# Kernel optimization log

Hardware: AMD Instinct MI355X
Metric: run time of the kernel (lower is better)

## Reference

```python
import jax, jax.numpy as jnp
import numpy as np

B, S, D, H = 2, 2048, 1024, 16
DH = D // H  # 64
NEG = -1000000000.0


def setup_inputs() -> dict:
    key = jax.random.key(0)
    ks = jax.random.split(key, 10)
    scale = 1.0 / np.sqrt(D)
    inp = {
        "x": jax.random.normal(ks[0], (B, S, D), dtype=jnp.float32),
        "mask": jax.random.randint(ks[1], (B, S, S), 0, 2, dtype=jnp.int32),
        "Wq": jax.random.normal(ks[2], (D, D), dtype=jnp.float32) * scale,
        "bq": jnp.zeros((D,), dtype=jnp.float32),
        "Wk": jax.random.normal(ks[3], (D, D), dtype=jnp.float32) * scale,
        "bk": jnp.zeros((D,), dtype=jnp.float32),
        "Wv": jax.random.normal(ks[4], (D, D), dtype=jnp.float32) * scale,
        "bv": jnp.zeros((D,), dtype=jnp.float32),
        "Wo": jax.random.normal(ks[5], (D, D), dtype=jnp.float32) * scale,
        "bo": jnp.zeros((D,), dtype=jnp.float32),
    }
    return inp


def reference(x, mask, Wq, bq, Wk, bk, Wv, bv, Wo, bo):
    b, s, _ = x.shape
    # Linear projections (torch Linear: y = x @ W^T + b), then split heads -> [b,h,s,dh]
    q = (x @ Wq.T + bq).reshape(b, s, H, DH).transpose(0, 2, 1, 3)
    k = (x @ Wk.T + bk).reshape(b, s, H, DH).transpose(0, 2, 1, 3)
    v = (x @ Wv.T + bv).reshape(b, s, H, DH).transpose(0, 2, 1, 3)
    # scores: [b,h,sq,sk]
    scores = jnp.einsum("bhqd,bhkd->bhqk", q, k) / jnp.sqrt(jnp.float32(DH))
    # code masks where mask == 0 (mask broadcast over heads)
    scores = jnp.where(mask[:, None, :, :] == 0, NEG, scores)
    attn = jax.nn.softmax(scores, axis=-1)
    out = jnp.einsum("bhqk,bhkd->bhqd", attn, v)  # [b,h,sq,dh]
    out = out.transpose(0, 2, 1, 3).reshape(b, s, D)  # merge heads -> [b,s,d]
    return out @ Wo.T + bo
```

## Files before the change

### kernel.cpp

```cpp
#include <hip/hip_runtime.h>
#include <stdint.h>

#define SB 2
#define SS 2048
#define SD 1024
#define SH 16
#define SDH 64
#define SM (SB*SS)
#define NEGINF_MASK -1000000000.0f
#define QSCALE 0.18033688011112043f

typedef __attribute__((ext_vector_type(8))) short short8;
typedef __attribute__((ext_vector_type(4))) short short4v;
typedef __attribute__((ext_vector_type(4))) float f32x4;
typedef __attribute__((ext_vector_type(4))) float float4v;
typedef __attribute__((ext_vector_type(2))) uint32_t uint2v;

__device__ static inline short f2bf(float f) {
    uint32_t u = __float_as_uint(f);
    u += 0x7fffu + ((u >> 16) & 1u);
    return (short)(u >> 16);
}

__device__ static inline void gload_lds16(const void* g, void* l) {
    __builtin_amdgcn_global_load_lds(
        (__attribute__((address_space(1))) void*)g,
        (__attribute__((address_space(3))) void*)l,
        16, 0, 0);
}

#define NX4 (SM*SD/4)
#define NW4 (SD*SD/4)
__global__ void cvt_all_kernel(const float* __restrict__ x,
                               const float* __restrict__ Wq, const float* __restrict__ Wk,
                               const float* __restrict__ Wv, const float* __restrict__ Wo,
                               short* __restrict__ xb,
                               short* __restrict__ wqb, short* __restrict__ wkb,
                               short* __restrict__ wvb, short* __restrict__ wob) {
    int i = blockIdx.x * 256 + threadIdx.x;
    const float* src; short* dst; int idx;
    if (i < NX4) { src = x; dst = xb; idx = i; }
    else {
        int j = i - NX4;
        int sel = j >> 18;
        idx = j & (NW4 - 1);
        src = (sel == 0) ? Wq : (sel == 1) ? Wk : (sel == 2) ? Wv : Wo;
        dst = (sel == 0) ? wqb : (sel == 1) ? wkb : (sel == 2) ? wvb : wob;
    }
    float4v v = *(const float4v*)(src + (size_t)idx * 4);
    short4v o;
    o[0] = f2bf(v[0]); o[1] = f2bf(v[1]); o[2] = f2bf(v[2]); o[3] = f2bf(v[3]);
    *(short4v*)(dst + (size_t)idx * 4) = o;
}

__global__ void pack_mask_kernel(const int* __restrict__ mask, unsigned long long* __restrict__ bits) {
    unsigned int i = blockIdx.x * 256u + threadIdx.x;
    int pred = mask[i] != 0;
    unsigned long long b = __ballot(pred);
    if ((threadIdx.x & 63u) == 0u) bits[i >> 6] = b;
}

template <typename OutT>
__device__ inline void gemm_bt_body(const short* __restrict__ A, const short* __restrict__ W,
                                    const float* __restrict__ bias, OutT* __restrict__ C,
                                    int M, int N, int K, int rowBase, int colBase, float scale) {
    __shared__ short As[2][128 * 32];
    __shared__ short Bs[2][128 * 32];
    const int tid = threadIdx.x, lane = tid & 63, wid = tid >> 6;
    const int r15 = lane & 15, hi = lane >> 4;
    const int wr = wid >> 1, wc = wid & 1;

    const int chBase0 = wid * 64, chBase1 = 256 + wid * 64;
    const int ch0 = chBase0 + lane, ch1 = chBase1 + lane;
    const short* aP0 = A + (size_t)(rowBase + (ch0 >> 2)) * K + (ch0 & 3) * 8;
    const short* aP1 = A + (size_t)(rowBase + (ch1 >> 2)) * K + (ch1 & 3) * 8;
    const short* bP0 = W + (size_t)(colBase + (ch0 >> 2)) * K + (ch0 & 3) * 8;
    const short* bP1 = W + (size_t)(colBase + (ch1 >> 2)) * K + (ch1 & 3) * 8;

    gload_lds16(aP0, &As[0][chBase0 * 8]);
    gload_lds16(aP1, &As[0][chBase1 * 8]);
    gload_lds16(bP0, &Bs[0][chBase0 * 8]);
    gload_lds16(bP1, &Bs[0][chBase1 * 8]);

    f32x4 acc[4][4] = {};
    const int NIT = K / 32;

    for (int it = 0; it < NIT; ++it) {
        __syncthreads();
        const int cur = it & 1, nxt = cur ^ 1;
        if (it + 1 < NIT) {
            int kt = (it + 1) * 32;
            gload_lds16(aP0 + kt, &As[nxt][chBase0 * 8]);
            gload_lds16(aP1 + kt, &As[nxt][chBase1 * 8]);
            gload_lds16(bP0 + kt, &Bs[nxt][chBase0 * 8]);
            gload_lds16(bP1 + kt, &Bs[nxt][chBase1 * 8]);
        }

        short8 aF[4], bF[4];
#pragma unroll
        for (int mi = 0; mi < 4; ++mi)
            aF[mi] = *(const short8*)&As[cur][(wr * 64 + mi * 16 + r15) * 32 + hi * 8];
#pragma unroll
        for (int ni = 0; ni < 4; ++ni)
            bF[ni] = *(const short8*)&Bs[cur][(wc * 64 + ni * 16 + r15) * 32 + hi * 8];

        __builtin_amdgcn_s_setprio(1);
#pragma unroll
        for (int mi = 0; mi < 4; ++mi)
#pragma unroll
            for (int ni = 0; ni < 4; ++ni)
                acc[mi][ni] = __builtin_amdgcn_mfma_f32_16x16x32_bf16(aF[mi], bF[ni], acc[mi][ni], 0, 0, 0);
        __builtin_amdgcn_s_setprio(0);
    }

#pragma unroll
    for (int ni = 0; ni < 4; ++ni) {
        int col = colBase + wc * 64 + ni * 16 + r15;
        float bv = bias[col];
#pragma unroll
        for (int mi = 0; mi < 4; ++mi) {
#pragma unroll
            for (int r = 0; r < 4; ++r) {
                int row = rowBase + wr * 64 + mi * 16 + hi * 4 + r;
                float v = (acc[mi][ni][r] + bv) * scale;
                if constexpr (sizeof(OutT) == 2) C[(size_t)row * N + col] = f2bf(v);
                else                             C[(size_t)row * N + col] = v;
            }
        }
    }
}

__global__ __launch_bounds__(256, 2) void gemm_qkv_kernel(
    const short* __restrict__ A,
    const short* __restrict__ W0, const short* __restrict__ W1, const short* __restrict__ W2,
    const float* __restrict__ b0, const float* __restrict__ b1, const float* __restrict__ b2,
    short* __restrict__ O0, short* __restrict__ O1, short* __restrict__ O2) {
    const short* W = (blockIdx.z == 0) ? W0 : (blockIdx.z == 1) ? W1 : W2;
    const float* bias = (blockIdx.z == 0) ? b0 : (blockIdx.z == 1) ? b1 : b2;
    short* C = (blockIdx.z == 0) ? O0 : (blockIdx.z == 1) ? O1 : O2;
    float scale = (blockIdx.z == 0) ? QSCALE : 1.0f;
    gemm_bt_body<short>(A, W, bias, C, SM, SD, SD, blockIdx.y * 128, blockIdx.x * 128, scale);
}

__global__ __launch_bounds__(256, 2) void gemm_out_kernel(
    const short* __restrict__ A, const short* __restrict__ W,
    const float* __restrict__ bias, float* __restrict__ C) {
    gemm_bt_body<float>(A, W, bias, C, SM, SD, SD, blockIdx.y * 128, blockIdx.x * 128, 1.0f);
}

__global__ __launch_bounds__(512, 4) void attn_kernel(
    const short* __restrict__ Q, const short* __restrict__ K, const short* __restrict__ V,
    const unsigned long long* __restrict__ mbits, short* __restrict__ O) {
    const int tid = threadIdx.x, lane = tid & 63, wid = tid >> 6;
    const int r15 = lane & 15, hi = lane >> 4;
    const int b = blockIdx.z, h = blockIdx.y;
    const int q0 = blockIdx.x * 128 + wid * 16;
    const int brow = b * SS;

    __shared__ short Ks[2][64 * 64];
    __shared__ short Vt[2][64 * 72];
    __shared__ short Pl[8][16 * 64];
    char* pw = (char*)&Pl[wid][0];

    const short* Kbase = K + (size_t)brow * SD + h * SDH;
    const short* Vbase = V + (size_t)brow * SD + h * SDH;
    const unsigned long long* mrow_p = mbits + (size_t)(brow + q0 + r15) * (SS / 64);

    short8 qF[2];
#pragma unroll
    for (int kd = 0; kd < 2; ++kd)
        qF[kd] = *(const short8*)&Q[(size_t)(brow + q0 + r15) * SD + h * SDH + kd * 32 + hi * 8];

    short8 onesF;
#pragma unroll
    for (int j = 0; j < 8; ++j) onesF[j] = (short)0x3F80;

    f32x4 o[4] = {};
    f32x4 lacc = {};
    float mrun = -1e30f;

    const int krow_s = tid >> 3, kcol_s = tid & 7;
    const int vp = tid & 31, vc0 = (tid >> 5) * 4;

    gload_lds16(Kbase + (size_t)krow_s * SD + ((kcol_s ^ (krow_s & 7)) * 8), &Ks[0][wid * 512]);
    short4v va = *(const short4v*)(Vbase + (size_t)(2 * vp) * SD + vc0);
    short4v vb2 = *(const short4v*)(Vbase + (size_t)(2 * vp + 1) * SD + vc0);
    unsigned long long mb = mrow_p[0];
#pragma unroll
    for (int j = 0; j < 4; ++j) {
        uint32_t pk = (uint32_t)(uint16_t)va[j] | ((uint32_t)(uint16_t)vb2[j] << 16);
        *(uint32_t*)&Vt[0][(vc0 + j) * 72 + 2 * vp] = pk;
    }

    for (int t = 0; t < SS / 64; ++t) {
        __syncthreads();
        const int cur = t & 1, nxt = cur ^ 1;
        const int tn = (t < SS / 64 - 1) ? t + 1 : t;

        gload_lds16(Kbase + (size_t)(tn * 64 + krow_s) * SD + ((kcol_s ^ (krow_s & 7)) * 8),
                    &Ks[nxt][wid * 512]);
        va  = *(const short4v*)(Vbase + (size_t)(tn * 64 + 2 * vp) * SD + vc0);
        vb2 = *(const short4v*)(Vbase + (size_t)(tn * 64 + 2 * vp + 1) * SD + vc0);
        unsigned long long mbn = mrow_p[tn];

        f32x4 s[4] = {};
        __builtin_amdgcn_s_setprio(1);
#pragma unroll
        for (int kc = 0; kc < 4; ++kc) {
            int krow = kc * 16 + r15;
#pragma unroll
            for (int kd = 0; kd < 2; ++kd) {
                short8 kF = *(const short8*)&Ks[cur][krow * 64 + (((kd * 4 + hi) ^ (krow & 7)) * 8)];
                s[kc] = __builtin_amdgcn_mfma_f32_16x16x32_bf16(kF, qF[kd], s[kc], 0, 0, 0);
            }
        }
        __builtin_amdgcn_s_setprio(0);

        float mloc = -1e30f;
#pragma unroll
        for (int kc = 0; kc < 4; ++kc) {
            unsigned nib = (unsigned)(mb >> (kc * 16 + hi * 4)) & 0xFu;
#pragma unroll
            for (int r = 0; r < 4; ++r) {
                float v = (nib & (1u << r)) ? s[kc][r] : NEGINF_MASK;
                s[kc][r] = v;
                mloc = fmaxf(mloc, v);
            }
        }
        mloc = fmaxf(mloc, __shfl_xor(mloc, 16));
        mloc = fmaxf(mloc, __shfl_xor(mloc, 32));

        if (__any(mloc > mrun + 8.f)) {
            float nm = fmaxf(mrun, mloc);
            float corr = exp2f(mrun - nm);
            mrun = nm;
            float cr[4];
#pragma unroll
            for (int r = 0; r < 4; ++r) cr[r] = __shfl(corr, hi * 4 + r);
#pragma unroll
            for (int r = 0; r < 4; ++r) lacc[r] *= cr[r];
#pragma unroll
            for (int df = 0; df < 4; ++df)
#pragma unroll
                for (int r = 0; r < 4; ++r) o[df][r] *= cr[r];
        }

#pragma unroll
        for (int kc = 0; kc < 4; ++kc)
#pragma unroll
            for (int r = 0; r < 4; ++r)
                s[kc][r] = exp2f(s[kc][r] - mrun);

#pragma unroll
        for (int kc = 0; kc < 4; ++kc) {
            uint32_t d0, d1;
            asm("v_cvt_pk_bf16_f32 %0, %1, %2" : "=v"(d0) : "v"(s[kc][0]), "v"(s[kc][1]));
            asm("v_cvt_pk_bf16_f32 %0, %1, %2" : "=v"(d1) : "v"(s[kc][2]), "v"(s[kc][3]));
            int chunk = (2 * kc + (hi >> 1)) ^ (r15 & 7);
            uint2v val = { d0, d1 };
            *(uint2v*)(pw + r15 * 128 + chunk * 16 + (hi & 1) * 8) = val;
        }

        short8 pF[2];
#pragma unroll
        for (int kf = 0; kf < 2; ++kf) {
            int chunk = (4 * kf + hi) ^ (r15 & 7);
            pF[kf] = *(const short8*)(pw + r15 * 128 + chunk * 16);
        }

        __builtin_amdgcn_s_setprio(1);
#pragma unroll
        for (int df = 0; df < 4; ++df) {
#pragma unroll
            for (int kf = 0; kf < 2; ++kf) {
                short8 vF = *(const short8*)&Vt[cur][(df * 16 + r15) * 72 + kf * 32 + hi * 8];
                o[df] = __builtin_amdgcn_mfma_f32_16x16x32_bf16(pF[kf], vF, o[df], 0, 0, 0);
            }
        }
        lacc = __builtin_amdgcn_mfma_f32_16x16x32_bf16(pF[0], onesF, lacc, 0, 0, 0);
        lacc = __builtin_amdgcn_mfma_f32_16x16x32_bf16(pF[1], onesF, lacc, 0, 0, 0);
        __builtin_amdgcn_s_setprio(0);

#pragma unroll
        for (int j = 0; j < 4; ++j) {
            uint32_t pk = (uint32_t)(uint16_t)va[j] | ((uint32_t)(uint16_t)vb2[j] << 16);
            *(uint32_t*)&Vt[nxt][(vc0 + j) * 72 + 2 * vp] = pk;
        }
        mb = mbn;
    }

#pragma unroll
    for (int r = 0; r < 4; ++r) {
        float inv = 1.0f / lacc[r];
        size_t row = (size_t)(brow + q0 + hi * 4 + r);
#pragma unroll
        for (int df = 0; df < 4; ++df)
            O[row * SD + h * SDH + df * 16 + r15] = f2bf(o[df][r] * inv);
    }
}

extern "C" void kernel_launch(void* const* d_in, const int* in_sizes, int n_in,
                              void* d_out, int out_size, void* d_ws, size_t ws_size,
                              hipStream_t stream) {
    const float* x  = (const float*)d_in[0];
    const int* mask = (const int*)d_in[1];
    const float* Wq = (const float*)d_in[2];
    const float* bq = (const float*)d_in[3];
    const float* Wk = (const float*)d_in[4];
    const float* bk = (const float*)d_in[5];
    const float* Wv = (const float*)d_in[6];
    const float* bv = (const float*)d_in[7];
    const float* Wo = (const float*)d_in[8];
    const float* bo = (const float*)d_in[9];
    float* out = (float*)d_out;

    char* ws = (char*)d_ws;
    size_t off = 0;
    auto alloc = [&](size_t bytes) { void* p = ws + off; off += (bytes + 255) & ~(size_t)255; return p; };

    short* xb  = (short*)alloc((size_t)SM * SD * 2);
    short* wqb = (short*)alloc((size_t)SD * SD * 2);
    short* wkb = (short*)alloc((size_t)SD * SD * 2);
    short* wvb = (short*)alloc((size_t)SD * SD * 2);
    short* wob = (short*)alloc((size_t)SD * SD * 2);
    short* Qb  = (short*)alloc((size_t)SM * SD * 2);
    short* Kb  = (short*)alloc((size_t)SM * SD * 2);
    short* Vb  = (short*)alloc((size_t)SM * SD * 2);
    short* AOb = (short*)alloc((size_t)SM * SD * 2);
    unsigned long long* mbits = (unsigned long long*)alloc((size_t)SB * SS * (SS / 64) * 8);

    cvt_all_kernel<<<(NX4 + 4 * NW4) / 256, 256, 0, stream>>>(
        x, Wq, Wk, Wv, Wo, xb, wqb, wkb, wvb, wob);
    pack_mask_kernel<<<SB * SS * SS / 256, 256, 0, stream>>>(mask, mbits);

    gemm_qkv_kernel<<<dim3(SD / 128, SM / 128, 3), 256, 0, stream>>>(
        xb, wqb, wkb, wvb, bq, bk, bv, Qb, Kb, Vb);

    attn_kernel<<<dim3(SS / 128, SH, SB), 512, 0, stream>>>(Qb, Kb, Vb, mbits, AOb);

    gemm_out_kernel<<<dim3(SD / 128, SM / 128), 256, 0, stream>>>(AOb, wob, bo, out);
}
```

Before: 161.3 us.

## Software-pipeline attention PV matmul behind next tile's QK with triple-buffered V

The attention loop now defers each tile's P·V and row-sum MFMAs to the next iteration, where they run right after that tile's QK^T MFMAs and before its softmax. This lets matrix work overlap with the exp and mask math. The V tile moves to a three-slot rotating LDS buffer, and a final P·V step runs after the loop. The QKV and output GEMM launch bounds are also raised to ask for three blocks per SIMD. The larger LDS footprint and the extra live registers for the held P fragments may lower attention occupancy.

```diff
diff --git a/kernel.cpp b/kernel.cpp
--- a/kernel.cpp
+++ b/kernel.cpp
@@ -130,7 +130,7 @@
     }
 }
 
-__global__ __launch_bounds__(256, 2) void gemm_qkv_kernel(
+__global__ __launch_bounds__(256, 3) void gemm_qkv_kernel(
     const short* __restrict__ A,
     const short* __restrict__ W0, const short* __restrict__ W1, const short* __restrict__ W2,
     const float* __restrict__ b0, const float* __restrict__ b1, const float* __restrict__ b2,
@@ -142,7 +142,7 @@
     gemm_bt_body<short>(A, W, bias, C, SM, SD, SD, blockIdx.y * 128, blockIdx.x * 128, scale);
 }
 
-__global__ __launch_bounds__(256, 2) void gemm_out_kernel(
+__global__ __launch_bounds__(256, 3) void gemm_out_kernel(
     const short* __restrict__ A, const short* __restrict__ W,
     const float* __restrict__ bias, float* __restrict__ C) {
     gemm_bt_body<float>(A, W, bias, C, SM, SD, SD, blockIdx.y * 128, blockIdx.x * 128, 1.0f);
@@ -156,9 +156,10 @@
     const int b = blockIdx.z, h = blockIdx.y;
     const int q0 = blockIdx.x * 128 + wid * 16;
     const int brow = b * SS;
+    const int NT = SS / 64;
 
     __shared__ short Ks[2][64 * 64];
-    __shared__ short Vt[2][64 * 72];
+    __shared__ short Vt[3][64 * 72];
     __shared__ short Pl[8][16 * 64];
     char* pw = (char*)&Pl[wid][0];
 
@@ -178,29 +179,32 @@
     f32x4 o[4] = {};
     f32x4 lacc = {};
     float mrun = -1e30f;
+    short8 pPrev[2] = {};
 
     const int krow_s = tid >> 3, kcol_s = tid & 7;
-    const int vp = tid & 31, vc0 = (tid >> 5) * 4;
+    const int vp_ = tid & 31, vc0 = (tid >> 5) * 4;
 
     gload_lds16(Kbase + (size_t)krow_s * SD + ((kcol_s ^ (krow_s & 7)) * 8), &Ks[0][wid * 512]);
-    short4v va = *(const short4v*)(Vbase + (size_t)(2 * vp) * SD + vc0);
-    short4v vb2 = *(const short4v*)(Vbase + (size_t)(2 * vp + 1) * SD + vc0);
+    short4v va = *(const short4v*)(Vbase + (size_t)(2 * vp_) * SD + vc0);
+    short4v vb2 = *(const short4v*)(Vbase + (size_t)(2 * vp_ + 1) * SD + vc0);
     unsigned long long mb = mrow_p[0];
 #pragma unroll
     for (int j = 0; j < 4; ++j) {
         uint32_t pk = (uint32_t)(uint16_t)va[j] | ((uint32_t)(uint16_t)vb2[j] << 16);
-        *(uint32_t*)&Vt[0][(vc0 + j) * 72 + 2 * vp] = pk;
-    }
-
-    for (int t = 0; t < SS / 64; ++t) {
+        *(uint32_t*)&Vt[0][(vc0 + j) * 72 + 2 * vp_] = pk;
+    }
+
+    int vbP = 2, vbC = 0, vbN = 1;
+
+    for (int t = 0; t < NT; ++t) {
         __syncthreads();
         const int cur = t & 1, nxt = cur ^ 1;
-        const int tn = (t < SS / 64 - 1) ? t + 1 : t;
+        const int tn = (t < NT - 1) ? t + 1 : t;
 
         gload_lds16(Kbase + (size_t)(tn * 64 + krow_s) * SD + ((kcol_s ^ (krow_s & 7)) * 8),
                     &Ks[nxt][wid * 512]);
-        va  = *(const short4v*)(Vbase + (size_t)(tn * 64 + 2 * vp) * SD + vc0);
-        vb2 = *(const short4v*)(Vbase + (size_t)(tn * 64 + 2 * vp + 1) * SD + vc0);
+        va  = *(const short4v*)(Vbase + (size_t)(tn * 64 + 2 * vp_) * SD + vc0);
+        vb2 = *(const short4v*)(Vbase + (size_t)(tn * 64 + 2 * vp_ + 1) * SD + vc0);
         unsigned long long mbn = mrow_p[tn];
 
         f32x4 s[4] = {};
@@ -213,6 +217,19 @@
                 short8 kF = *(const short8*)&Ks[cur][krow * 64 + (((kd * 4 + hi) ^ (krow & 7)) * 8)];
                 s[kc] = __builtin_amdgcn_mfma_f32_16x16x32_bf16(kF, qF[kd], s[kc], 0, 0, 0);
             }
+        }
+
+        if (t) {
+#pragma unroll
+            for (int df = 0; df < 4; ++df) {
+#pragma unroll
+                for (int kf = 0; kf < 2; ++kf) {
+                    short8 vF = *(const short8*)&Vt[vbP][(df * 16 + r15) * 72 + kf * 32 + hi * 8];
+                    o[df] = __builtin_amdgcn_mfma_f32_16x16x32_bf16(pPrev[kf], vF, o[df], 0, 0, 0);
+                }
+            }
+            lacc = __builtin_amdgcn_mfma_f32_16x16x32_bf16(pPrev[0], onesF, lacc, 0, 0, 0);
+            lacc = __builtin_amdgcn_mfma_f32_16x16x32_bf16(pPrev[1], onesF, lacc, 0, 0, 0);
         }
         __builtin_amdgcn_s_setprio(0);
 
@@ -261,33 +278,31 @@
             *(uint2v*)(pw + r15 * 128 + chunk * 16 + (hi & 1) * 8) = val;
         }
 
-        short8 pF[2];
 #pragma unroll
         for (int kf = 0; kf < 2; ++kf) {
             int chunk = (4 * kf + hi) ^ (r15 & 7);
-            pF[kf] = *(const short8*)(pw + r15 * 128 + chunk * 16);
-        }
-
-        __builtin_amdgcn_s_setprio(1);
-#pragma unroll
-        for (int df = 0; df < 4; ++df) {
-#pragma unroll
-            for (int kf = 0; kf < 2; ++kf) {
-                short8 vF = *(const short8*)&Vt[cur][(df * 16 + r15) * 72 + kf * 32 + hi * 8];
-                o[df] = __builtin_amdgcn_mfma_f32_16x16x32_bf16(pF[kf], vF, o[df], 0, 0, 0);
-            }
-        }
-        lacc = __builtin_amdgcn_mfma_f32_16x16x32_bf16(pF[0], onesF, lacc, 0, 0, 0);
-        lacc = __builtin_amdgcn_mfma_f32_16x16x32_bf16(pF[1], onesF, lacc, 0, 0, 0);
-        __builtin_amdgcn_s_setprio(0);
+            pPrev[kf] = *(const short8*)(pw + r15 * 128 + chunk * 16);
+        }
 
 #pragma unroll
         for (int j = 0; j < 4; ++j) {
             uint32_t pk = (uint32_t)(uint16_t)va[j] | ((uint32_t)(uint16_t)vb2[j] << 16);
-            *(uint32_t*)&Vt[nxt][(vc0 + j) * 72 + 2 * vp] = pk;
+            *(uint32_t*)&Vt[vbN][(vc0 + j) * 72 + 2 * vp_] = pk;
         }
         mb = mbn;
-    }
+        int tmp = vbP; vbP = vbC; vbC = vbN; vbN = tmp;
+    }
+
+#pragma unroll
+    for (int df = 0; df < 4; ++df) {
+#pragma unroll
+        for (int kf = 0; kf < 2; ++kf) {
+            short8 vF = *(const short8*)&Vt[vbP][(df * 16 + r15) * 72 + kf * 32 + hi * 8];
+            o[df] = __builtin_amdgcn_mfma_f32_16x16x32_bf16(pPrev[kf], vF, o[df], 0, 0, 0);
+        }
+    }
+    lacc = __builtin_amdgcn_mfma_f32_16x16x32_bf16(pPrev[0], onesF, lacc, 0, 0, 0);
+    lacc = __builtin_amdgcn_mfma_f32_16x16x32_bf16(pPrev[1], onesF, lacc, 0, 0, 0);
 
 #pragma unroll
     for (int r = 0; r < 4; ++r) {
```

New measurement: 164.3 us. About the same (+1.8%).
